# Optimization experiments

Hardware: AMD Instinct MI355X
Metric: run time of the kernel (lower is better)

## Reference

```python
import jax, jax.numpy as jnp
import numpy as np

B, C, D = 4, 1024, 1024
H, DH = 16, 64  # num_heads, head_size; D == H*DH


def setup_inputs() -> dict:
    key = jax.random.key(0)
    ks = jax.random.split(key, 8)
    return {
        "query_input": jax.random.normal(ks[0], (B, C, D), dtype=jnp.float32),
        "key_input": jax.random.normal(ks[1], (B, C, D), dtype=jnp.float32),
        "value_input": jax.random.normal(ks[2], (B, C, D), dtype=jnp.float32),
        "Wq": jax.random.normal(ks[3], (D, D), dtype=jnp.float32) * 0.02,
        "Wk": jax.random.normal(ks[4], (D, D), dtype=jnp.float32) * 0.02,
        "Wv": jax.random.normal(ks[5], (D, D), dtype=jnp.float32) * 0.02,
        "Wp": jax.random.normal(ks[6], (D, D), dtype=jnp.float32) * 0.02,
        "bp": jax.random.normal(ks[7], (D,), dtype=jnp.float32) * 0.02,
        "mask": jnp.zeros((C, C), dtype=bool),
    }


def _split_heads(x):
    # (B, C, D) -> (B, H, C, DH)
    return x.reshape(B, C, H, DH).transpose(0, 2, 1, 3)


def reference(query_input, key_input, value_input, Wq, Wk, Wv, Wp, bp, mask):
    scale = DH ** -0.5
    q = _split_heads(query_input @ Wq.T)
    k = _split_heads(key_input @ Wk.T)
    v = _split_heads(value_input @ Wv.T)
    # ||q_i - k_j||_2 via norm decomposition: |q|^2 + |k|^2 - 2 q.k
    q2 = jnp.sum(q * q, axis=-1)  # (B, H, C)
    k2 = jnp.sum(k * k, axis=-1)  # (B, H, C)
    qk = jnp.einsum("bhqd,bhkd->bhqk", q, k)  # (B, H, C, C)
    sq = jnp.maximum(q2[..., :, None] + k2[..., None, :] - 2.0 * qk, 0.0)
    wei = jnp.sqrt(sq) * scale
    wei = jnp.where(mask, -jnp.inf, wei)
    wei = jax.nn.softmax(wei, axis=-1)
    out = jnp.einsum("bhqk,bhkd->bhqd", wei, v)  # (B, H, C, DH)
    out = out.transpose(0, 2, 1, 3).reshape(B, C, D)
    return out @ Wp.T + bp
```

## Files before the change

### kernel.cpp

```cpp
#include <hip/hip_runtime.h>


typedef _Float16 f16;
typedef __attribute__((ext_vector_type(2))) _Float16 f16x2;
typedef __attribute__((ext_vector_type(8))) _Float16 f16x8;
typedef __attribute__((ext_vector_type(4))) float f32x4;

#define MFMA16(a, b, c) __builtin_amdgcn_mfma_f32_16x16x32_f16((a), (b), (c), 0, 0, 0)

constexpr double LOG2E = 1.4426950408889634;
constexpr double C2d = 0.015625 * LOG2E * LOG2E;

#if __has_builtin(__builtin_amdgcn_exp2f)
#define EXP2F(x) __builtin_amdgcn_exp2f(x)
#else
#define EXP2F(x) exp2f(x)
#endif
#if __has_builtin(__builtin_amdgcn_sqrtf)
#define SQRTF(x) __builtin_amdgcn_sqrtf(x)
#else
#define SQRTF(x) sqrtf(x)
#endif

__device__ __forceinline__ void stage16(const f16* g, f16* lds_base_uniform) {
#if __has_builtin(__builtin_amdgcn_global_load_lds)
    __builtin_amdgcn_global_load_lds((const __attribute__((address_space(1))) void*)g,
                                     (__attribute__((address_space(3))) void*)lds_base_uniform,
                                     16, 0, 0);
#else
    const int lane = threadIdx.x & 63;
    *(f16x8*)(lds_base_uniform + lane * 8) = *(const f16x8*)g;
#endif
}

__global__ __launch_bounds__(256) void cvt_all(const float* __restrict__ Xq,
                                               const float* __restrict__ Xk,
                                               const float* __restrict__ Xv,
                                               const float* __restrict__ Wq,
                                               const float* __restrict__ Wk,
                                               const float* __restrict__ Wv,
                                               const float* __restrict__ Wp,
                                               f16* __restrict__ W16,
                                               f16* __restrict__ X16) {
    const size_t idx = (size_t)blockIdx.x * 2048 + threadIdx.x * 8;
    const size_t M4 = 4ull << 20, M1 = 1ull << 20;
    const float* s;
    f16* d;
    if (idx < 3 * M4) {
        if (idx < M4) s = Xq + idx;
        else if (idx < 2 * M4) s = Xk + (idx - M4);
        else s = Xv + (idx - 2 * M4);
        d = X16 + idx;
    } else {
        size_t wi = idx - 3 * M4;
        if (wi < M1) s = Wq + wi;
        else if (wi < 2 * M1) s = Wk + (wi - M1);
        else if (wi < 3 * M1) s = Wv + (wi - 2 * M1);
        else s = Wp + (wi - 3 * M1);
        d = W16 + wi;
    }
    float4 a = *(const float4*)s;
    float4 b = *(const float4*)(s + 4);
    f16x8 o;
    o[0] = (f16)a.x; o[1] = (f16)a.y; o[2] = (f16)a.z; o[3] = (f16)a.w;
    o[4] = (f16)b.x; o[5] = (f16)b.y; o[6] = (f16)b.z; o[7] = (f16)b.w;
    *(f16x8*)d = o;
}

template <bool NORMS, bool F32OUT>
__global__ __launch_bounds__(256, 2) void gemm_bt(const f16* __restrict__ A,
                                                  const f16* __restrict__ Bw,
                                                  f16* __restrict__ Co,
                                                  float* __restrict__ Cf,
                                                  const float* __restrict__ bias,
                                                  float* __restrict__ nrm,
                                                  float osc0, float osc1,
                                                  float ns0, float ns1,
                                                  int M, int N, int K) {
    __shared__ __attribute__((aligned(16))) f16 As[128 * 64];
    __shared__ __attribute__((aligned(16))) f16 Bs[64 * 64];
    const int tid = threadIdx.x;
    const int lane = tid & 63;
    const int w = tid >> 6;
    const int l15 = lane & 15, l4 = lane >> 4;
    const int z = blockIdx.z;
    A += (size_t)z * (4u << 20);
    Bw += (size_t)z * (1u << 20);
    Co += (size_t)z * (4u << 20);
    if (NORMS) nrm += (size_t)z * 65536;
    const float osc = z ? osc1 : osc0;
    const float nscale = z ? ns1 : ns0;
    const int wr = w * 32;
    const int nwg = gridDim.x * gridDim.y;
    const int f = blockIdx.y * gridDim.x + blockIdx.x;
    const int g = (f & 7) * (nwg >> 3) + (f >> 3);
    const int row0 = (g / gridDim.x) * 128;
    const int col0 = (g % gridDim.x) * 64;

    const int sr8 = lane >> 3;
    const int sc8 = (lane & 7) * 8;
    f32x4 acc[2][4] = {};

    for (int kt = 0; kt < K; kt += 64) {
        __syncthreads();
#pragma unroll
        for (int t = 0; t < 4; ++t)
            stage16(&A[(size_t)(row0 + w * 32 + t * 8 + sr8) * K + kt + sc8], &As[(w * 32 + t * 8) * 64]);
#pragma unroll
        for (int t = 0; t < 2; ++t)
            stage16(&Bw[(size_t)(col0 + w * 16 + t * 8 + sr8) * K + kt + sc8], &Bs[(w * 16 + t * 8) * 64]);
        __syncthreads();
#pragma unroll
        for (int ks = 0; ks < 2; ++ks) {
            f16x8 af[2], bf[4];
#pragma unroll
            for (int m = 0; m < 2; ++m)
                af[m] = *(const f16x8*)&As[(wr + m * 16 + l15) * 64 + ks * 32 + l4 * 8];
#pragma unroll
            for (int n = 0; n < 4; ++n)
                bf[n] = *(const f16x8*)&Bs[(n * 16 + l15) * 64 + ks * 32 + l4 * 8];
#pragma unroll
            for (int m = 0; m < 2; ++m)
#pragma unroll
                for (int n = 0; n < 4; ++n) acc[m][n] = MFMA16(af[m], bf[n], acc[m][n]);
        }
    }

    if (NORMS) {
        const int h = col0 >> 6;
#pragma unroll
        for (int m = 0; m < 2; ++m)
#pragma unroll
            for (int r = 0; r < 4; ++r) {
                float s = 0.f;
#pragma unroll
                for (int n = 0; n < 4; ++n) {
                    float v = (float)(f16)(acc[m][n][r] * osc);
                    s += v * v;
                }
                s += __shfl_xor(s, 1);
                s += __shfl_xor(s, 2);
                s += __shfl_xor(s, 4);
                s += __shfl_xor(s, 8);
                if (l15 == 0) {
                    int row = row0 + wr + m * 16 + l4 * 4 + r;
                    nrm[(size_t)((row >> 10) * 16 + h) * 1024 + (row & 1023)] = s * nscale;
                }
            }
    }

#pragma unroll
    for (int m = 0; m < 2; ++m)
#pragma unroll
        for (int n = 0; n < 4; ++n)
#pragma unroll
            for (int r = 0; r < 4; ++r) {
                int rr = row0 + wr + m * 16 + l4 * 4 + r;
                int cc = col0 + n * 16 + l15;
                if (F32OUT)
                    Cf[(size_t)rr * N + cc] = acc[m][n][r] + bias[cc];
                else
                    Co[(size_t)rr * N + cc] = (f16)(acc[m][n][r] * osc);
            }
}

__global__ __launch_bounds__(256, 2) void attn(const f16* __restrict__ qs,
                                               const f16* __restrict__ kb,
                                               const f16* __restrict__ vT,
                                               const float* __restrict__ q2c2,
                                               const float* __restrict__ k2c2,
                                               f16* __restrict__ out) {
    __shared__ __attribute__((aligned(16))) f16 Ks[128 * 64];
    __shared__ __attribute__((aligned(16))) f16 Vs[64 * 128];
    __shared__ float k2tile[128];
    const int tid = threadIdx.x;
    const int lane = tid & 63;
    const int w = tid >> 6;
    const int l15 = lane & 15, l4 = lane >> 4;
    const int fid = blockIdx.y * 8 + blockIdx.x;
    const int qt = (fid >> 3) & 7;
    const int bh = (fid & 7) * 8 + (fid >> 6);
    const int b = bh >> 4, h = bh & 15;
    const int wq = w * 32;
    const int hcol = h * 64;
    const int qrow0 = b * 1024 + qt * 128;
    const f16* vTh = vT + (size_t)hcol * 4096 + b * 1024;

    const int sr = tid >> 3, sc0 = (tid & 7) * 8;
    const int vr = tid >> 4, vc0 = (tid & 15) * 8;
    const int vsw = (vr & 7) << 3;
    const int fsw = (l15 & 7) << 3;

    f16x8 bq[2][2];
#pragma unroll
    for (int m = 0; m < 2; ++m)
#pragma unroll
        for (int ks = 0; ks < 2; ++ks)
            bq[m][ks] = *(const f16x8*)&qs[(size_t)(qrow0 + wq + m * 16 + l15) * 1024 + hcol + ks * 32 + l4 * 8];
    float q2m[2];
#pragma unroll
    for (int m = 0; m < 2; ++m) q2m[m] = q2c2[(size_t)bh * 1024 + qt * 128 + wq + m * 16 + l15];

    f32x4 accv[2][4] = {};
    float den[2] = {0.f, 0.f};

    f16x8 kreg[4], vreg[4];
    float k2reg = 0.f;
#define ISSUE_LOADS(KT)                                                                                      \
    {                                                                                                        \
        _Pragma("unroll") for (int i = 0; i < 4; ++i)                                                        \
            kreg[i] = *(const f16x8*)&kb[(size_t)(b * 1024 + (KT) * 128 + sr + i * 32) * 1024 + hcol + sc0]; \
        _Pragma("unroll") for (int j = 0; j < 4; ++j)                                                        \
            vreg[j] = *(const f16x8*)&vTh[(size_t)(vr + j * 16) * 4096 + (KT) * 128 + vc0];                  \
        k2reg = (tid < 128) ? k2c2[(size_t)bh * 1024 + (KT) * 128 + tid] : 0.f;                              \
    }

    ISSUE_LOADS(0)

    for (int kt = 0; kt < 8; ++kt) {
        __syncthreads();
#pragma unroll
        for (int i = 0; i < 4; ++i) {
            const int kap = sr + i * 32;
            const int s = ((kap >> 5) & 3) * 32 + ((kap >> 2) & 1) * 16 + ((kap >> 3) & 3) * 4 + (kap & 3);
            *(f16x8*)&Ks[s * 64 + (sc0 ^ ((s & 7) << 3))] = kreg[i];
        }
#pragma unroll
        for (int j = 0; j < 4; ++j) *(f16x8*)&Vs[(vr + j * 16) * 128 + (vc0 ^ vsw)] = vreg[j];
        if (tid < 128) k2tile[tid] = k2reg;
        __syncthreads();
        if (kt < 7) ISSUE_LOADS(kt + 1)

#pragma unroll
        for (int kk = 0; kk < 4; ++kk) {
            unsigned um[2][4];
#pragma unroll
            for (int half = 0; half < 2; ++half) {
                const int n = kk * 2 + half;
                f16x8 kf0 = *(const f16x8*)&Ks[(n * 16 + l15) * 64 + ((l4 * 8) ^ fsw)];
                f16x8 kf1 = *(const f16x8*)&Ks[(n * 16 + l15) * 64 + ((32 + l4 * 8) ^ fsw)];
                f32x4 k2q = *(const f32x4*)&k2tile[kk * 32 + l4 * 8 + half * 4];
#pragma unroll
                for (int m = 0; m < 2; ++m) {
                    f32x4 c0;
#pragma unroll
                    for (int r = 0; r < 4; ++r) c0[r] = q2m[m] + k2q[r];
                    f32x4 st = MFMA16(kf0, bq[m][0], c0);
                    st = MFMA16(kf1, bq[m][1], st);
                    float p0 = EXP2F(SQRTF(fmaxf(st[0], 0.f)));
                    float p1 = EXP2F(SQRTF(fmaxf(st[1], 0.f)));
                    float p2 = EXP2F(SQRTF(fmaxf(st[2], 0.f)));
                    float p3 = EXP2F(SQRTF(fmaxf(st[3], 0.f)));
                    den[m] += (p0 + p1) + (p2 + p3);
                    f16x2 lo = {(f16)p0, (f16)p1};
                    f16x2 hi = {(f16)p2, (f16)p3};
                    um[m][half * 2] = __builtin_bit_cast(unsigned, lo);
                    um[m][half * 2 + 1] = __builtin_bit_cast(unsigned, hi);
                }
            }
            f16x8 ap[2];
#pragma unroll
            for (int m = 0; m < 2; ++m) {
                uint4 u = {um[m][0], um[m][1], um[m][2], um[m][3]};
                ap[m] = __builtin_bit_cast(f16x8, u);
            }
#pragma unroll
            for (int n2 = 0; n2 < 4; ++n2) {
                f16x8 bv = *(const f16x8*)&Vs[(n2 * 16 + l15) * 128 + ((kk * 32 + l4 * 8) ^ fsw)];
#pragma unroll
                for (int m = 0; m < 2; ++m) accv[m][n2] = MFMA16(ap[m], bv, accv[m][n2]);
            }
        }
    }

    float iden[2];
#pragma unroll
    for (int m = 0; m < 2; ++m) {
        float d = den[m];
        d += __shfl_xor(d, 16);
        d += __shfl_xor(d, 32);
        iden[m] = 1.0f / d;
    }
#pragma unroll
    for (int m = 0; m < 2; ++m)
#pragma unroll
        for (int r = 0; r < 4; ++r) {
            const float rd = __shfl(iden[m], l4 * 4 + r);
#pragma unroll
            for (int n2 = 0; n2 < 4; ++n2)
                out[(size_t)(qrow0 + wq + m * 16 + l4 * 4 + r) * 1024 + hcol + n2 * 16 + l15] =
                    (f16)(accv[m][n2][r] * rd);
        }
}

extern "C" void kernel_launch(void* const* d_in, const int* in_sizes, int n_in,
                              void* d_out, int out_size, void* d_ws, size_t ws_size,
                              hipStream_t stream) {
    const float* Xq = (const float*)d_in[0];
    const float* Xk = (const float*)d_in[1];
    const float* Xv = (const float*)d_in[2];
    const float* Wq = (const float*)d_in[3];
    const float* Wk = (const float*)d_in[4];
    const float* Wv = (const float*)d_in[5];
    const float* Wp = (const float*)d_in[6];
    const float* bp = (const float*)d_in[7];
    float* out = (float*)d_out;

    char* ws = (char*)d_ws;
    f16* W16 = (f16*)(ws);
    f16* X16 = (f16*)(ws + (8ull << 20));
    f16* vTb = (f16*)(ws + (8ull << 20));
    f16* attnout = (f16*)(ws + (16ull << 20));
    f16* Xv16 = (f16*)(ws + (24ull << 20));
    f16* qb = (f16*)(ws + (32ull << 20));
    f16* kb = (f16*)(ws + (40ull << 20));
    float* q2c2 = out;
    float* k2c2 = out + 65536;

    const float qsc = (float)(-2.0 * C2d);
    const float ns_q = (float)(1.0 / (4.0 * C2d));
    const float ns_k = (float)C2d;

    cvt_all<<<8192, 256, 0, stream>>>(Xq, Xk, Xv, Wq, Wk, Wv, Wp, W16, X16);

    gemm_bt<true, false><<<dim3(16, 32, 2), 256, 0, stream>>>(
        X16, W16, qb, nullptr, nullptr, q2c2, qsc, 1.0f, ns_q, ns_k, 4096, 1024, 1024);

    gemm_bt<false, false><<<dim3(64, 8), 256, 0, stream>>>(
        W16 + 2 * (1u << 20), Xv16, vTb, nullptr, nullptr, nullptr, 1.0f, 1.0f, 0.f, 0.f, 1024, 4096, 1024);

    attn<<<dim3(8, 64), 256, 0, stream>>>(qb, kb, vTb, q2c2, k2c2, attnout);

    gemm_bt<false, true><<<dim3(16, 32), 256, 0, stream>>>(
        attnout, W16 + 3 * (1u << 20), nullptr, out, bp, nullptr, 1.0f, 1.0f, 0.f, 0.f, 4096, 1024, 1024);
}
```

Measured before the change: 121.7 us.

## Use 128x128 tiles with 32x32 MFMA and swizzled LDS; MFMA row sums

The GEMM kernel moves from a 128x64 block tile built on 16x16x32 MFMA to a 128x128 tile built on 32x32x16 MFMA. Each wave now computes a 64x64 sub-tile, and an XOR swizzle on the LDS staging avoids bank conflicts. This raises data reuse per load and cuts grid sizes in half. Separately, the attention kernel drops the per-lane scalar denominator sum and shuffle reduction and computes the softmax row sums with an extra MFMA against a ones vector. That sum now comes from f16-rounded probabilities, which may slightly change accuracy.

```diff
diff --git a/kernel.cpp b/kernel.cpp
--- a/kernel.cpp
+++ b/kernel.cpp
@@ -5,8 +5,10 @@
 typedef __attribute__((ext_vector_type(2))) _Float16 f16x2;
 typedef __attribute__((ext_vector_type(8))) _Float16 f16x8;
 typedef __attribute__((ext_vector_type(4))) float f32x4;
+typedef __attribute__((ext_vector_type(16))) float f32x16;
 
 #define MFMA16(a, b, c) __builtin_amdgcn_mfma_f32_16x16x32_f16((a), (b), (c), 0, 0, 0)
+#define MFMA32(a, b, c) __builtin_amdgcn_mfma_f32_32x32x16_f16((a), (b), (c), 0, 0, 0)
 
 constexpr double LOG2E = 1.4426950408889634;
 constexpr double C2d = 0.015625 * LOG2E * LOG2E;
@@ -22,15 +24,22 @@
 #define SQRTF(x) sqrtf(x)
 #endif
 
-__device__ __forceinline__ void stage16(const f16* g, f16* lds_base_uniform) {
+__device__ __forceinline__ void stage16(const void* g, void* lds_base_uniform) {
 #if __has_builtin(__builtin_amdgcn_global_load_lds)
     __builtin_amdgcn_global_load_lds((const __attribute__((address_space(1))) void*)g,
                                      (__attribute__((address_space(3))) void*)lds_base_uniform,
                                      16, 0, 0);
 #else
     const int lane = threadIdx.x & 63;
-    *(f16x8*)(lds_base_uniform + lane * 8) = *(const f16x8*)g;
+    *(f16x8*)((f16*)lds_base_uniform + lane * 8) = *(const f16x8*)g;
 #endif
+}
+
+__device__ __forceinline__ f16x8 cvt8v(f32x4 a, f32x4 b) {
+    f16x8 o;
+    o[0] = (f16)a[0]; o[1] = (f16)a[1]; o[2] = (f16)a[2]; o[3] = (f16)a[3];
+    o[4] = (f16)b[0]; o[5] = (f16)b[1]; o[6] = (f16)b[2]; o[7] = (f16)b[3];
+    return o;
 }
 
 __global__ __launch_bounds__(256) void cvt_all(const float* __restrict__ Xq,
@@ -59,109 +68,102 @@
         else s = Wp + (wi - 3 * M1);
         d = W16 + wi;
     }
-    float4 a = *(const float4*)s;
-    float4 b = *(const float4*)(s + 4);
-    f16x8 o;
-    o[0] = (f16)a.x; o[1] = (f16)a.y; o[2] = (f16)a.z; o[3] = (f16)a.w;
-    o[4] = (f16)b.x; o[5] = (f16)b.y; o[6] = (f16)b.z; o[7] = (f16)b.w;
-    *(f16x8*)d = o;
-}
-
-template <bool NORMS, bool F32OUT>
-__global__ __launch_bounds__(256, 2) void gemm_bt(const f16* __restrict__ A,
-                                                  const f16* __restrict__ Bw,
-                                                  f16* __restrict__ Co,
-                                                  float* __restrict__ Cf,
-                                                  const float* __restrict__ bias,
-                                                  float* __restrict__ nrm,
-                                                  float osc0, float osc1,
-                                                  float ns0, float ns1,
-                                                  int M, int N, int K) {
+    f32x4 a = *(const f32x4*)s;
+    f32x4 b = *(const f32x4*)(s + 4);
+    *(f16x8*)d = cvt8v(a, b);
+}
+
+template <int MODE>
+__global__ __launch_bounds__(256, 2) void gemm(const f16* __restrict__ A,
+                                               const f16* __restrict__ B,
+                                               f16* __restrict__ Co,
+                                               float* __restrict__ Cf,
+                                               const float* __restrict__ bias,
+                                               float* __restrict__ nrm,
+                                               float osc0, float osc1,
+                                               float ns0, float ns1,
+                                               int M, int N, int K) {
+    constexpr bool NORMS = (MODE == 0);
+    constexpr bool F32OUT = (MODE == 2);
     __shared__ __attribute__((aligned(16))) f16 As[128 * 64];
-    __shared__ __attribute__((aligned(16))) f16 Bs[64 * 64];
+    __shared__ __attribute__((aligned(16))) f16 Bs[128 * 64];
     const int tid = threadIdx.x;
     const int lane = tid & 63;
     const int w = tid >> 6;
-    const int l15 = lane & 15, l4 = lane >> 4;
+    const int l31 = lane & 31, l5 = lane >> 5;
     const int z = blockIdx.z;
-    A += (size_t)z * (4u << 20);
-    Bw += (size_t)z * (1u << 20);
-    Co += (size_t)z * (4u << 20);
-    if (NORMS) nrm += (size_t)z * 65536;
+    const f16* Ap = (MODE == 0) ? A + (size_t)z * (4u << 20) : A;
+    const f16* Bp = (MODE == 0) ? B + (size_t)z * (1u << 20) : B;
+    f16* Cop = (MODE == 0) ? Co + (size_t)z * (4u << 20) : Co;
+    float* nrmp = NORMS ? nrm + (size_t)z * 65536 : nullptr;
     const float osc = z ? osc1 : osc0;
     const float nscale = z ? ns1 : ns0;
-    const int wr = w * 32;
+    const int wr = (w >> 1) * 64, wc = (w & 1) * 64;
     const int nwg = gridDim.x * gridDim.y;
     const int f = blockIdx.y * gridDim.x + blockIdx.x;
     const int g = (f & 7) * (nwg >> 3) + (f >> 3);
     const int row0 = (g / gridDim.x) * 128;
-    const int col0 = (g % gridDim.x) * 64;
-
-    const int sr8 = lane >> 3;
-    const int sc8 = (lane & 7) * 8;
-    f32x4 acc[2][4] = {};
+    const int col0 = (g % gridDim.x) * 128;
+
+    f32x16 acc[2][2] = {};
 
     for (int kt = 0; kt < K; kt += 64) {
         __syncthreads();
 #pragma unroll
-        for (int t = 0; t < 4; ++t)
-            stage16(&A[(size_t)(row0 + w * 32 + t * 8 + sr8) * K + kt + sc8], &As[(w * 32 + t * 8) * 64]);
-#pragma unroll
-        for (int t = 0; t < 2; ++t)
-            stage16(&Bw[(size_t)(col0 + w * 16 + t * 8 + sr8) * K + kt + sc8], &Bs[(w * 16 + t * 8) * 64]);
+        for (int t = 0; t < 4; ++t) {
+            const int rb = w * 32 + t * 8;
+            const int rr = rb + (lane >> 3);
+            const int gs = (lane & 7) ^ (rr & 7);
+            stage16(&Ap[(size_t)(row0 + rr) * K + kt + gs * 8], &As[rb * 64]);
+            stage16(&Bp[(size_t)(col0 + rr) * K + kt + gs * 8], &Bs[rb * 64]);
+        }
         __syncthreads();
 #pragma unroll
-        for (int ks = 0; ks < 2; ++ks) {
-            f16x8 af[2], bf[4];
-#pragma unroll
-            for (int m = 0; m < 2; ++m)
-                af[m] = *(const f16x8*)&As[(wr + m * 16 + l15) * 64 + ks * 32 + l4 * 8];
-#pragma unroll
-            for (int n = 0; n < 4; ++n)
-                bf[n] = *(const f16x8*)&Bs[(n * 16 + l15) * 64 + ks * 32 + l4 * 8];
-#pragma unroll
-            for (int m = 0; m < 2; ++m)
-#pragma unroll
-                for (int n = 0; n < 4; ++n) acc[m][n] = MFMA16(af[m], bf[n], acc[m][n]);
+        for (int ks = 0; ks < 4; ++ks) {
+            const int gq = ks * 2 + l5;
+            f16x8 af[2], bf[2];
+#pragma unroll
+            for (int mr = 0; mr < 2; ++mr)
+                af[mr] = *(const f16x8*)&As[(wr + mr * 32 + l31) * 64 + ((gq ^ (l31 & 7)) * 8)];
+#pragma unroll
+            for (int n2 = 0; n2 < 2; ++n2)
+                bf[n2] = *(const f16x8*)&Bs[(wc + n2 * 32 + l31) * 64 + ((gq ^ (l31 & 7)) * 8)];
+#pragma unroll
+            for (int mr = 0; mr < 2; ++mr)
+#pragma unroll
+                for (int n2 = 0; n2 < 2; ++n2) acc[mr][n2] = MFMA32(af[mr], bf[n2], acc[mr][n2]);
         }
     }
 
-    if (NORMS) {
-        const int h = col0 >> 6;
-#pragma unroll
-        for (int m = 0; m < 2; ++m)
-#pragma unroll
-            for (int r = 0; r < 4; ++r) {
-                float s = 0.f;
-#pragma unroll
-                for (int n = 0; n < 4; ++n) {
-                    float v = (float)(f16)(acc[m][n][r] * osc);
-                    s += v * v;
+    const int cc0 = col0 + wc + l31;
+    const int cc1 = col0 + wc + 32 + l31;
+    const int hh = (col0 + wc) >> 6;
+#pragma unroll
+    for (int mr = 0; mr < 2; ++mr)
+#pragma unroll
+        for (int j = 0; j < 16; ++j) {
+            const int rr = row0 + wr + mr * 32 + (j & 3) + 8 * (j >> 2) + 4 * l5;
+            if (F32OUT) {
+                Cf[(size_t)rr * N + cc0] = acc[mr][0][j] + bias[cc0];
+                Cf[(size_t)rr * N + cc1] = acc[mr][1][j] + bias[cc1];
+            } else {
+                const f16 h0 = (f16)(acc[mr][0][j] * osc);
+                const f16 h1 = (f16)(acc[mr][1][j] * osc);
+                if (NORMS) {
+                    float v0 = (float)h0, v1 = (float)h1;
+                    float s = v0 * v0 + v1 * v1;
+                    s += __shfl_xor(s, 1);
+                    s += __shfl_xor(s, 2);
+                    s += __shfl_xor(s, 4);
+                    s += __shfl_xor(s, 8);
+                    s += __shfl_xor(s, 16);
+                    if (l31 == 0)
+                        nrmp[(size_t)((rr >> 10) * 16 + hh) * 1024 + (rr & 1023)] = s * nscale;
                 }
-                s += __shfl_xor(s, 1);
-                s += __shfl_xor(s, 2);
-                s += __shfl_xor(s, 4);
-                s += __shfl_xor(s, 8);
-                if (l15 == 0) {
-                    int row = row0 + wr + m * 16 + l4 * 4 + r;
-                    nrm[(size_t)((row >> 10) * 16 + h) * 1024 + (row & 1023)] = s * nscale;
-                }
+                Cop[(size_t)rr * N + cc0] = h0;
+                Cop[(size_t)rr * N + cc1] = h1;
             }
-    }
-
-#pragma unroll
-    for (int m = 0; m < 2; ++m)
-#pragma unroll
-        for (int n = 0; n < 4; ++n)
-#pragma unroll
-            for (int r = 0; r < 4; ++r) {
-                int rr = row0 + wr + m * 16 + l4 * 4 + r;
-                int cc = col0 + n * 16 + l15;
-                if (F32OUT)
-                    Cf[(size_t)rr * N + cc] = acc[m][n][r] + bias[cc];
-                else
-                    Co[(size_t)rr * N + cc] = (f16)(acc[m][n][r] * osc);
-            }
+        }
 }
 
 __global__ __launch_bounds__(256, 2) void attn(const f16* __restrict__ qs,
@@ -202,7 +204,9 @@
     for (int m = 0; m < 2; ++m) q2m[m] = q2c2[(size_t)bh * 1024 + qt * 128 + wq + m * 16 + l15];
 
     f32x4 accv[2][4] = {};
-    float den[2] = {0.f, 0.f};
+    f32x4 dacc[2] = {};
+    const f16 one = (f16)1.f;
+    const f16x8 ones8 = {one, one, one, one, one, one, one, one};
 
     f16x8 kreg[4], vreg[4];
     float k2reg = 0.f;
@@ -251,7 +255,6 @@
                     float p1 = EXP2F(SQRTF(fmaxf(st[1], 0.f)));
                     float p2 = EXP2F(SQRTF(fmaxf(st[2], 0.f)));
                     float p3 = EXP2F(SQRTF(fmaxf(st[3], 0.f)));
-                    den[m] += (p0 + p1) + (p2 + p3);
                     f16x2 lo = {(f16)p0, (f16)p1};
                     f16x2 hi = {(f16)p2, (f16)p3};
                     um[m][half * 2] = __builtin_bit_cast(unsigned, lo);
@@ -265,6 +268,8 @@
                 ap[m] = __builtin_bit_cast(f16x8, u);
             }
 #pragma unroll
+            for (int m = 0; m < 2; ++m) dacc[m] = MFMA16(ap[m], ones8, dacc[m]);
+#pragma unroll
             for (int n2 = 0; n2 < 4; ++n2) {
                 f16x8 bv = *(const f16x8*)&Vs[(n2 * 16 + l15) * 128 + ((kk * 32 + l4 * 8) ^ fsw)];
 #pragma unroll
@@ -273,19 +278,11 @@
         }
     }
 
-    float iden[2];
-#pragma unroll
-    for (int m = 0; m < 2; ++m) {
-        float d = den[m];
-        d += __shfl_xor(d, 16);
-        d += __shfl_xor(d, 32);
-        iden[m] = 1.0f / d;
-    }
 #pragma unroll
     for (int m = 0; m < 2; ++m)
 #pragma unroll
         for (int r = 0; r < 4; ++r) {
-            const float rd = __shfl(iden[m], l4 * 4 + r);
+            const float rd = 1.0f / dacc[m][r];
 #pragma unroll
             for (int n2 = 0; n2 < 4; ++n2)
                 out[(size_t)(qrow0 + wq + m * 16 + l4 * 4 + r) * 1024 + hcol + n2 * 16 + l15] =
@@ -323,14 +320,16 @@
 
     cvt_all<<<8192, 256, 0, stream>>>(Xq, Xk, Xv, Wq, Wk, Wv, Wp, W16, X16);
 
-    gemm_bt<true, false><<<dim3(16, 32, 2), 256, 0, stream>>>(
+    gemm<0><<<dim3(8, 32, 2), 256, 0, stream>>>(
         X16, W16, qb, nullptr, nullptr, q2c2, qsc, 1.0f, ns_q, ns_k, 4096, 1024, 1024);
 
-    gemm_bt<false, false><<<dim3(64, 8), 256, 0, stream>>>(
-        W16 + 2 * (1u << 20), Xv16, vTb, nullptr, nullptr, nullptr, 1.0f, 1.0f, 0.f, 0.f, 1024, 4096, 1024);
+    gemm<1><<<dim3(32, 8), 256, 0, stream>>>(
+        W16 + 2 * (1u << 20), Xv16, vTb, nullptr, nullptr, nullptr,
+        1.0f, 1.0f, 0.f, 0.f, 1024, 4096, 1024);
 
     attn<<<dim3(8, 64), 256, 0, stream>>>(qb, kb, vTb, q2c2, k2c2, attnout);
 
-    gemm_bt<false, true><<<dim3(16, 32), 256, 0, stream>>>(
-        attnout, W16 + 3 * (1u << 20), nullptr, out, bp, nullptr, 1.0f, 1.0f, 0.f, 0.f, 4096, 1024, 1024);
-}
+    gemm<2><<<dim3(8, 32), 256, 0, stream>>>(
+        attnout, W16 + 3 * (1u << 20), nullptr, out, bp, nullptr,
+        1.0f, 1.0f, 0.f, 0.f, 4096, 1024, 1024);
+}
```

Result: faster. 119.3 us (-2.0%).
